# Performance work log

Measured on AMD Instinct MI355X. Metric: run time of the kernel, lower is better.

The kernel has to match this reference:

```python
import jax, jax.numpy as jnp
import numpy as np

H = 24        # attn.heads (Flux)
ENC = 512     # encoder (text) token count, hard-coded in the source via emb[:512]
EPS = 1e-6    # RMSNorm eps


def _rms(x, w):
    # RMSNorm over head_dim (Flux norm_q / norm_k)
    return x * jax.lax.rsqrt(jnp.mean(x * x, axis=-1, keepdims=True) + EPS) * w


def _rope(x, cos, sin):
    # diffusers apply_rotary_emb, use_real=True, unbind_dim=-1
    xr = x.reshape(x.shape[:-1] + (-1, 2))
    rot = jnp.stack([-xr[..., 1], xr[..., 0]], axis=-1).reshape(x.shape)
    return x * cos + rot * sin


def setup_inputs() -> dict:
    key = jax.random.key(0)
    ks = jax.random.split(key, 26)
    B, F, D = 2, 1024, 3072
    hd = D // H
    S = ENC + F
    lin = lambda k: 0.02 * jax.random.normal(k, (D, D), jnp.float32)
    bias = lambda k: 0.02 * jax.random.normal(k, (D,), jnp.float32)
    nw = lambda k: 1.0 + 0.02 * jax.random.normal(k, (hd,), jnp.float32)
    return {
        'hidden_states': jax.random.normal(ks[0], (B, F, D), jnp.float32),
        'encoder_hidden_states': jax.random.normal(ks[1], (B, ENC, D), jnp.float32),
        'rot_cos': jax.random.uniform(ks[2], (S, hd), jnp.float32, minval=-1.0, maxval=1.0),
        'rot_sin': jax.random.uniform(ks[3], (S, hd), jnp.float32, minval=-1.0, maxval=1.0),
        'wq': lin(ks[4]), 'bq': bias(ks[5]),
        'wk': lin(ks[6]), 'bk': bias(ks[7]),
        'wv': lin(ks[8]), 'bv': bias(ks[9]),
        'waq': lin(ks[10]), 'baq': bias(ks[11]),
        'wak': lin(ks[12]), 'bak': bias(ks[13]),
        'wav': lin(ks[14]), 'bav': bias(ks[15]),
        'wo': lin(ks[16]), 'bo': bias(ks[17]),
        'wao': lin(ks[18]), 'bao': bias(ks[19]),
        'nq': nw(ks[20]), 'nk': nw(ks[21]),
        'naq': nw(ks[22]), 'nak': nw(ks[23]),
    }


def reference(hidden_states, encoder_hidden_states, rot_cos, rot_sin,
              wq, bq, wk, bk, wv, bv, waq, baq, wak, bak, wav, bav,
              wo, bo, wao, bao, nq, nk, naq, nak):
    B, F, D = hidden_states.shape
    hd = D // H

    def proj(x, w, b):
        y = x @ w.T + b
        return y.reshape(x.shape[0], -1, H, hd).transpose(0, 2, 1, 3)  # [B,H,S,hd]

    q = _rms(proj(hidden_states, wq, bq), nq)   # [B,H,F,hd]
    k = _rms(proj(hidden_states, wk, bk), nk)
    v = proj(hidden_states, wv, bv)

    # cross-batch mixing: 'b h f d -> 1 h (b f) d' then repeat over batch
    k = jnp.broadcast_to(k.transpose(1, 0, 2, 3).reshape(1, H, B * F, hd), (B, H, B * F, hd))
    v = jnp.broadcast_to(v.transpose(1, 0, 2, 3).reshape(1, H, B * F, hd), (B, H, B * F, hd))

    # key rotary: encoder part once, image part repeated num_components times
    cos_k = jnp.concatenate([rot_cos[:ENC]] + [rot_cos[ENC:]] * B, axis=0)
    sin_k = jnp.concatenate([rot_sin[:ENC]] + [rot_sin[ENC:]] * B, axis=0)

    eq = _rms(proj(encoder_hidden_states, waq, baq), naq)  # [B,H,ENC,hd]
    ek = _rms(proj(encoder_hidden_states, wak, bak), nak)
    ev = proj(encoder_hidden_states, wav, bav)

    q = jnp.concatenate([eq, q], axis=2)  # [B,H,ENC+F,hd]
    k = jnp.concatenate([ek, k], axis=2)  # [B,H,ENC+B*F,hd]
    v = jnp.concatenate([ev, v], axis=2)

    q = _rope(q, rot_cos, rot_sin)
    k = _rope(k, cos_k, sin_k)

    scale = hd ** -0.5
    attn = jax.nn.softmax(jnp.einsum('bhqd,bhkd->bhqk', q, k) * scale, axis=-1)
    out = jnp.einsum('bhqk,bhkd->bhqd', attn, v)
    out = out.transpose(0, 2, 1, 3).reshape(B, -1, D)  # [B,ENC+F,D]

    enc_out = out[:, :ENC] @ wao.T + bao
    hs_out = out[:, ENC:] @ wo.T + bo
    return (hs_out, enc_out)
```

## Files before the change

### kernel.cpp

```cpp
#include <hip/hip_runtime.h>

typedef __attribute__((ext_vector_type(8))) short bf16x8;
typedef __attribute__((ext_vector_type(8))) unsigned short u16x8;
typedef __attribute__((ext_vector_type(4))) unsigned short u16x4;
typedef __attribute__((ext_vector_type(4))) float f32x4;

#define DEV static __device__ __forceinline__

DEV unsigned short f2bf(float f){
  unsigned u = __float_as_uint(f);
  u += 0x7fff + ((u>>16)&1);
  return (unsigned short)(u>>16);
}
DEV float bf2f(unsigned short b){ return __uint_as_float(((unsigned)b)<<16); }

DEV void gll16(const void* g, void* l){
  __builtin_amdgcn_global_load_lds((__attribute__((address_space(1))) unsigned*)(void*)g,
                                   (__attribute__((address_space(3))) unsigned*)l, 16, 0, 0);
}

__global__ void k_cast(const float* __restrict__ x, unsigned short* __restrict__ y, int n4){
  int i = blockIdx.x*256 + threadIdx.x;
  if (i >= n4) return;
  f32x4 v = ((const f32x4*)x)[i];
  u16x4 o = { f2bf(v.x), f2bf(v.y), f2bf(v.z), f2bf(v.w) };
  ((u16x4*)y)[i] = o;
}

__global__ __launch_bounds__(256) void k_gemm(
    const unsigned short* __restrict__ X, const unsigned short* __restrict__ W,
    unsigned short* __restrict__ Yb, float* __restrict__ Yf,
    const float* __restrict__ ba, const float* __restrict__ bb, const float* __restrict__ bc,
    int N, int K, int sec_nb, int tpb_log2, int stot, int soff)
{
  __shared__ unsigned short As[2][4096];
  __shared__ unsigned short Bs[2][4096];
  const int t = threadIdx.x, w = t>>6, l = t&63;
  const int by = blockIdx.y;
  const int wsel = (by >= 2*sec_nb) ? 2 : (by >= sec_nb ? 1 : 0);
  const int Cl = (by - wsel*sec_nb)*128;
  const unsigned short* Wp = W + (long)wsel*sec_nb*128*K;
  const float* bias = (wsel==0) ? ba : (wsel==1 ? bb : bc);
  const int R = blockIdx.x*128, C = by*128;
  const long xbase = (long)(R>>tpb_log2)*stot + soff + (R & ((1<<tpb_log2)-1));
  const int wr = w>>1, wc = w&1;
  f32x4 acc[4][4] = {};
  const int nk = K>>5;

  auto stage = [&](int buf, int kt){
    const int k0 = kt*32;
    #pragma unroll
    for (int c=0;c<2;c++){
      int row = c*64 + (t>>2);
      int scol = ((t&3)<<3) ^ ((row&3)<<3);
      gll16(X + (xbase+row)*K + k0 + scol, &As[buf][c*2048 + w*512]);
      gll16(Wp + (long)(Cl+row)*K + k0 + scol, &Bs[buf][c*2048 + w*512]);
    }
  };

  stage(0,0);
  int buf = 0;
  for (int kt=0; kt<nk; kt++){
    __syncthreads();
    if (kt+1 < nk) stage(buf^1, kt+1);
    bf16x8 a[4], b[4];
    #pragma unroll
    for (int m=0;m<4;m++){
      int ar = wr*64 + m*16 + (l&15);
      int ac = ((l>>4)<<3) ^ ((ar&3)<<3);
      a[m] = *(const bf16x8*)&As[buf][ar*32 + ac];
      int br = wc*64 + m*16 + (l&15);
      int bc2 = ((l>>4)<<3) ^ ((br&3)<<3);
      b[m] = *(const bf16x8*)&Bs[buf][br*32 + bc2];
    }
    #pragma unroll
    for (int m=0;m<4;m++)
      #pragma unroll
      for (int n=0;n<4;n++)
        acc[m][n] = __builtin_amdgcn_mfma_f32_16x16x32_bf16(a[m], b[n], acc[m][n], 0,0,0);
    buf ^= 1;
  }

  #pragma unroll
  for (int m=0;m<4;m++){
    int row = R + wr*64 + m*16 + ((l>>4)<<2);
    #pragma unroll
    for (int n=0;n<4;n++){
      int cl = wc*64 + n*16 + (l&15);
      float bvv = bias[Cl + cl];
      int col = C + cl;
      #pragma unroll
      for (int r=0;r<4;r++){
        float v = acc[m][n][r] + bvv;
        long idx = (long)(row+r)*N + col;
        if (Yf) Yf[idx] = v;
        else Yb[idx] = f2bf(v);
      }
    }
  }
}

__global__ __launch_bounds__(256) void k_gemmO(
    const unsigned short* __restrict__ X, const unsigned short* __restrict__ Wf,
    float* __restrict__ out, const float* __restrict__ bo, const float* __restrict__ bao)
{
  const int K = 3072;
  __shared__ unsigned short As[2][4096];
  __shared__ unsigned short Bs[2][4096];
  const int t = threadIdx.x, w = t>>6, l = t&63;
  const int bx = blockIdx.x, by = blockIdx.y;
  const bool enc = bx >= 16;
  const unsigned short* Wp = Wf + (enc ? 9437184 : 0);
  const float* bias = enc ? bao : bo;
  const int R = bx*128, C = by*128;
  long xbase, obase;
  if (!enc){ xbase = (long)(R>>10)*1536 + 512 + (R&1023); obase = (long)R*3072; }
  else { int Rp = R-2048; xbase = (long)(Rp>>9)*1536 + (Rp&511); obase = 6291456 + (long)Rp*3072; }
  const int wr = w>>1, wc = w&1;
  f32x4 acc[4][4] = {};

  auto stage = [&](int buf, int kt){
    const int k0 = kt*32;
    #pragma unroll
    for (int c=0;c<2;c++){
      int row = c*64 + (t>>2);
      int scol = ((t&3)<<3) ^ ((row&3)<<3);
      gll16(X + (xbase+row)*K + k0 + scol, &As[buf][c*2048 + w*512]);
      gll16(Wp + (long)(C+row)*K + k0 + scol, &Bs[buf][c*2048 + w*512]);
    }
  };

  stage(0,0);
  int buf = 0;
  for (int kt=0; kt<96; kt++){
    __syncthreads();
    if (kt+1 < 96) stage(buf^1, kt+1);
    bf16x8 a[4], b[4];
    #pragma unroll
    for (int m=0;m<4;m++){
      int ar = wr*64 + m*16 + (l&15);
      int ac = ((l>>4)<<3) ^ ((ar&3)<<3);
      a[m] = *(const bf16x8*)&As[buf][ar*32 + ac];
      int br = wc*64 + m*16 + (l&15);
      int bc2 = ((l>>4)<<3) ^ ((br&3)<<3);
      b[m] = *(const bf16x8*)&Bs[buf][br*32 + bc2];
    }
    #pragma unroll
    for (int m=0;m<4;m++)
      #pragma unroll
      for (int n=0;n<4;n++)
        acc[m][n] = __builtin_amdgcn_mfma_f32_16x16x32_bf16(a[m], b[n], acc[m][n], 0,0,0);
    buf ^= 1;
  }

  #pragma unroll
  for (int m=0;m<4;m++){
    int rl = wr*64 + m*16 + ((l>>4)<<2);
    #pragma unroll
    for (int n=0;n<4;n++){
      int col = C + wc*64 + n*16 + (l&15);
      float bvv = bias[col];
      #pragma unroll
      for (int r=0;r<4;r++)
        out[obase + (long)(rl+r)*3072 + col] = acc[m][n][r] + bvv;
    }
  }
}

__global__ void k_ppqk(const unsigned short* __restrict__ Y, int ystr, int yoff,
    const float* __restrict__ nw,
    const float* __restrict__ cs, const float* __restrict__ sn, unsigned short* __restrict__ dst,
    int T_log2, int tpb_log2, int dest_off, int S, int no_batch,
    int pos_off, int pos_mask, float qscale)
{
  int rid = blockIdx.x*4 + (threadIdx.x>>6);
  int l = threadIdx.x & 63;
  int h = rid >> T_log2, tk = rid & ((1<<T_log2)-1);
  unsigned pair = *(const unsigned*)(Y + (long)tk*ystr + yoff + h*128 + 2*l);
  float x0 = bf2f((unsigned short)(pair&0xffff));
  float x1 = bf2f((unsigned short)(pair>>16));
  float ss = x0*x0 + x1*x1;
  #pragma unroll
  for (int m=1;m<64;m<<=1) ss += __shfl_xor(ss, m);
  float rr = rsqrtf(ss*(1.0f/128.0f) + 1e-6f);
  x0 *= rr*nw[2*l]; x1 *= rr*nw[2*l+1];
  int p = pos_off + (tk & pos_mask);
  float c0 = cs[p*128 + 2*l], c1 = cs[p*128 + 2*l+1];
  float s0 = sn[p*128 + 2*l], s1 = sn[p*128 + 2*l+1];
  float o0 = (x0*c0 - x1*s0)*qscale;
  float o1 = (x1*c1 + x0*s1)*qscale;
  long idx;
  if (no_batch) idx = (long)h*S + tk;
  else {
    int b = tk >> tpb_log2;
    int sq = dest_off + (tk & ((1<<tpb_log2)-1));
    idx = (long)(b*24+h)*S + sq;
  }
  unsigned out = (unsigned)f2bf(o0) | ((unsigned)f2bf(o1)<<16);
  *(unsigned*)(dst + idx*128 + 2*l) = out;
}

__global__ void k_ppv(const unsigned short* __restrict__ Y, int ystr, int yoff,
                      unsigned short* __restrict__ Vt, int vstr, int no_batch)
{
  __shared__ unsigned short tileS[64][136];
  int t = threadIdx.x, h = blockIdx.y;
  int tile0 = blockIdx.x*64;
  #pragma unroll
  for (int c=0;c<4;c++){
    int j = c*16 + (t>>4), col = (t&15)*8;
    *(u16x8*)&tileS[j][col] = *(const u16x8*)(Y + (long)(tile0+j)*ystr + yoff + h*128 + col);
  }
  __syncthreads();
  int d = t>>1, half = t&1;
  unsigned short tmp[32];
  #pragma unroll
  for (int i=0;i<32;i++) tmp[i] = tileS[half*32+i][d];
  long base;
  if (no_batch) base = ((long)h*128 + d)*vstr + tile0 + half*32;
  else { int b = tile0>>9; base = ((long)(b*24+h)*128 + d)*vstr + (tile0&511) + half*32; }
  #pragma unroll
  for (int k=0;k<4;k++) *(u16x8*)(Vt + base + k*8) = *(const u16x8*)&tmp[k*8];
}

__global__ __launch_bounds__(256) void k_attn(
    const unsigned short* __restrict__ Q,
    const unsigned short* __restrict__ Ke, const unsigned short* __restrict__ Ki,
    const unsigned short* __restrict__ Ve, const unsigned short* __restrict__ Vi,
    unsigned short* __restrict__ AO)
{
  __shared__ unsigned short Ks[8192];
  __shared__ unsigned short Vs[8192];
  __shared__ unsigned short Ps[4][1408];
  const int t = threadIdx.x, w = t>>6, l = t&63;
  const int h = blockIdx.y, b = blockIdx.z;
  const int bh = b*24 + h;
  const int q0 = blockIdx.x*64 + w*16;

  bf16x8 qf[4];
  {
    const unsigned short* qp = Q + ((long)bh*1536 + q0 + (l&15))*128 + ((l>>4)<<3);
    #pragma unroll
    for (int kc=0;kc<4;kc++) qf[kc] = *(const bf16x8*)(qp + kc*32);
  }
  f32x4 o[8] = {};
  float mx[4] = {-1e30f,-1e30f,-1e30f,-1e30f};
  float ls[4] = {0,0,0,0};

  for (int jt=0; jt<40; jt++){
    const unsigned short *ksrc, *vsrc; int vstr;
    if (jt < 8){
      ksrc = Ke + ((long)bh*512 + jt*64)*128;
      vsrc = Ve + (long)bh*65536 + jt*64;
      vstr = 512;
    } else {
      ksrc = Ki + ((long)h*2048 + (jt-8)*64)*128;
      vsrc = Vi + (long)h*262144 + (jt-8)*64;
      vstr = 2048;
    }
    #pragma unroll
    for (int c=0;c<4;c++){
      int row = c*16 + (t>>4);
      int col = ((t&15)<<3) ^ ((row&7)<<3);
      gll16(ksrc + row*128 + col, &Ks[c*2048 + w*512]);
    }
    #pragma unroll
    for (int c=0;c<4;c++){
      int row = c*32 + (t>>3);
      int col = ((t&7)<<3) ^ ((row&7)<<3);
      gll16(vsrc + (long)row*vstr + col, &Vs[c*2048 + w*512]);
    }
    __syncthreads();

    f32x4 sf[4];
    __builtin_amdgcn_s_setprio(1);
    #pragma unroll
    for (int ct=0;ct<4;ct++){
      f32x4 s = {};
      #pragma unroll
      for (int kc=0;kc<4;kc++){
        int krow = ct*16 + (l&15);
        int kcol = (kc*32 + ((l>>4)<<3)) ^ ((krow&7)<<3);
        bf16x8 kb = *(const bf16x8*)&Ks[krow*128 + kcol];
        s = __builtin_amdgcn_mfma_f32_16x16x32_bf16(qf[kc], kb, s, 0,0,0);
      }
      sf[ct] = s;
    }
    __builtin_amdgcn_s_setprio(0);

    float pm[4]; int ok = 1;
    #pragma unroll
    for (int r=0;r<4;r++){
      pm[r] = fmaxf(fmaxf(sf[0][r],sf[1][r]), fmaxf(sf[2][r],sf[3][r]));
      ok &= (pm[r] <= mx[r] + 8.0f);
    }
    if (!__all(ok)){
      #pragma unroll
      for (int r=0;r<4;r++){
        float tmax = pm[r];
        #pragma unroll
        for (int m=1;m<16;m<<=1) tmax = fmaxf(tmax, __shfl_xor(tmax, m));
        float mn = fmaxf(mx[r], tmax);
        float al = exp2f(mx[r]-mn);
        mx[r] = mn;
        ls[r] *= al;
        #pragma unroll
        for (int f=0;f<8;f++) o[f][r] *= al;
      }
    }
    #pragma unroll
    for (int ct=0;ct<4;ct++){
      #pragma unroll
      for (int r=0;r<4;r++){
        float pv = exp2f(sf[ct][r]-mx[r]);
        ls[r] += pv;
        int prow = ((l>>4)<<2) + r;
        Ps[w][prow*88 + ct*16 + (l&15)] = f2bf(pv);
      }
    }
    bf16x8 pa[2];
    #pragma unroll
    for (int kc=0;kc<2;kc++)
      pa[kc] = *(const bf16x8*)&Ps[w][(l&15)*88 + kc*32 + ((l>>4)<<3)];
    __builtin_amdgcn_s_setprio(1);
    #pragma unroll
    for (int f=0;f<8;f++){
      #pragma unroll
      for (int kc=0;kc<2;kc++){
        int vrow = f*16 + (l&15);
        int vcol = (kc*32 + ((l>>4)<<3)) ^ ((vrow&7)<<3);
        bf16x8 vb = *(const bf16x8*)&Vs[vrow*64 + vcol];
        o[f] = __builtin_amdgcn_mfma_f32_16x16x32_bf16(pa[kc], vb, o[f], 0,0,0);
      }
    }
    __builtin_amdgcn_s_setprio(0);
    __syncthreads();
  }

  #pragma unroll
  for (int r=0;r<4;r++){
    #pragma unroll
    for (int m=1;m<16;m<<=1) ls[r] += __shfl_xor(ls[r], m);
  }
  #pragma unroll
  for (int r=0;r<4;r++){
    int qrow = q0 + ((l>>4)<<2) + r;
    float inv = 1.0f/ls[r];
    #pragma unroll
    for (int f=0;f<8;f++){
      AO[((long)b*1536 + qrow)*3072 + h*128 + f*16 + (l&15)] = f2bf(o[f][r]*inv);
    }
  }
}

extern "C" void kernel_launch(void* const* d_in, const int* in_sizes, int n_in,
                              void* d_out, int out_size, void* d_ws, size_t ws_size,
                              hipStream_t stream)
{
  const float* hs  = (const float*)d_in[0];
  const float* ehs = (const float*)d_in[1];
  const float* rc  = (const float*)d_in[2];
  const float* rs_ = (const float*)d_in[3];
  const float* wq = (const float*)d_in[4];  const float* bq = (const float*)d_in[5];
  const float* wk = (const float*)d_in[6];  const float* bk = (const float*)d_in[7];
  const float* wv = (const float*)d_in[8];  const float* bv = (const float*)d_in[9];
  const float* waq= (const float*)d_in[10]; const float* baq= (const float*)d_in[11];
  const float* wak= (const float*)d_in[12]; const float* bak= (const float*)d_in[13];
  const float* wav= (const float*)d_in[14]; const float* bav= (const float*)d_in[15];
  const float* wo = (const float*)d_in[16]; const float* bo = (const float*)d_in[17];
  const float* wao= (const float*)d_in[18]; const float* bao= (const float*)d_in[19];
  const float* nq = (const float*)d_in[20]; const float* nk = (const float*)d_in[21];
  const float* naq= (const float*)d_in[22]; const float* nak= (const float*)d_in[23];

  const float qsc = (float)(0.08838834764831845 * 1.4426950408889634);

  char* p = (char*)d_ws;
  auto alloc = [&](size_t bytes){ char* r = p; p += bytes; return r; };

  if (ws_size >= (size_t)169869312){
    unsigned short* Xh = (unsigned short*)alloc(12582912);
    unsigned short* Xe = (unsigned short*)alloc(6291456);
    unsigned short* Wb = (unsigned short*)alloc(56623104);
    unsigned short* Yb = (unsigned short*)alloc(37748736);
    unsigned short* Qb = (unsigned short*)alloc(18874368);
    unsigned short* Ke = (unsigned short*)alloc(6291456);
    unsigned short* Ki = (unsigned short*)alloc(12582912);
    unsigned short* Ve = (unsigned short*)alloc(6291456);
    unsigned short* Vi = (unsigned short*)alloc(12582912);
    unsigned short* AO = Xh;

    k_cast<<<6144,256,0,stream>>>(hs, Xh, 1572864);
    k_cast<<<3072,256,0,stream>>>(ehs, Xe, 786432);

    k_cast<<<9216,256,0,stream>>>(wq, Wb, 2359296);
    k_cast<<<9216,256,0,stream>>>(wk, Wb + 9437184, 2359296);
    k_cast<<<9216,256,0,stream>>>(wv, Wb + 18874368, 2359296);
    k_gemm<<<dim3(16,72),256,0,stream>>>(Xh, Wb, Yb, nullptr, bq, bk, bv, 9216,3072, 24, 20,0,0);
    k_ppqk<<<12288,256,0,stream>>>(Yb, 9216, 0,    nq, rc, rs_, Qb, 11, 10, 512, 1536, 0, 512, 1023, qsc);
    k_ppqk<<<12288,256,0,stream>>>(Yb, 9216, 3072, nk, rc, rs_, Ki, 11, 0,  0,   2048, 1, 512, 1023, 1.0f);
    k_ppv<<<dim3(32,24),256,0,stream>>>(Yb, 9216, 6144, Vi, 2048, 1);

    k_cast<<<9216,256,0,stream>>>(waq, Wb, 2359296);
    k_cast<<<9216,256,0,stream>>>(wak, Wb + 9437184, 2359296);
    k_cast<<<9216,256,0,stream>>>(wav, Wb + 18874368, 2359296);
    k_gemm<<<dim3(8,72),256,0,stream>>>(Xe, Wb, Yb, nullptr, baq, bak, bav, 9216,3072, 24, 20,0,0);
    k_ppqk<<<6144,256,0,stream>>>(Yb, 9216, 0,    naq, rc, rs_, Qb, 10, 9, 0, 1536, 0, 0, 511, qsc);
    k_ppqk<<<6144,256,0,stream>>>(Yb, 9216, 3072, nak, rc, rs_, Ke, 10, 9, 0, 512,  0, 0, 511, 1.0f);
    k_ppv<<<dim3(16,24),256,0,stream>>>(Yb, 9216, 6144, Ve, 512, 0);

    k_attn<<<dim3(24,24,2),256,0,stream>>>(Qb, Ke, Ki, Ve, Vi, AO);

    k_cast<<<9216,256,0,stream>>>(wo,  Wb, 2359296);
    k_cast<<<9216,256,0,stream>>>(wao, Wb + 9437184, 2359296);
    k_gemmO<<<dim3(24,24),256,0,stream>>>(AO, Wb, (float*)d_out, bo, bao);
  } else {
    unsigned short* Xh = (unsigned short*)alloc(12582912);
    unsigned short* Xe = (unsigned short*)alloc(6291456);
    unsigned short* Wb = (unsigned short*)alloc(18874368);
    unsigned short* Yb = (unsigned short*)alloc(12582912);
    unsigned short* Qb = (unsigned short*)alloc(18874368);
    unsigned short* Ke = (unsigned short*)alloc(6291456);
    unsigned short* Ki = (unsigned short*)alloc(12582912);
    unsigned short* Ve = (unsigned short*)alloc(6291456);
    unsigned short* Vi = (unsigned short*)alloc(12582912);
    unsigned short* AO = Xh;

    k_cast<<<6144,256,0,stream>>>(hs, Xh, 1572864);
    k_cast<<<3072,256,0,stream>>>(ehs, Xe, 786432);
    auto cW = [&](const float* ww){ k_cast<<<9216,256,0,stream>>>(ww, Wb, 2359296); };

    cW(wq);
    k_gemm<<<dim3(16,24),256,0,stream>>>(Xh, Wb, Yb, nullptr, bq,bq,bq, 3072,3072, 24, 20,0,0);
    k_ppqk<<<12288,256,0,stream>>>(Yb, 3072, 0, nq, rc, rs_, Qb, 11, 10, 512, 1536, 0, 512, 1023, qsc);
    cW(wk);
    k_gemm<<<dim3(16,24),256,0,stream>>>(Xh, Wb, Yb, nullptr, bk,bk,bk, 3072,3072, 24, 20,0,0);
    k_ppqk<<<12288,256,0,stream>>>(Yb, 3072, 0, nk, rc, rs_, Ki, 11, 0, 0, 2048, 1, 512, 1023, 1.0f);
    cW(wv);
    k_gemm<<<dim3(16,24),256,0,stream>>>(Xh, Wb, Yb, nullptr, bv,bv,bv, 3072,3072, 24, 20,0,0);
    k_ppv<<<dim3(32,24),256,0,stream>>>(Yb, 3072, 0, Vi, 2048, 1);

    cW(waq);
    k_gemm<<<dim3(8,24),256,0,stream>>>(Xe, Wb, Yb, nullptr, baq,baq,baq, 3072,3072, 24, 20,0,0);
    k_ppqk<<<6144,256,0,stream>>>(Yb, 3072, 0, naq, rc, rs_, Qb, 10, 9, 0, 1536, 0, 0, 511, qsc);
    cW(wak);
    k_gemm<<<dim3(8,24),256,0,stream>>>(Xe, Wb, Yb, nullptr, bak,bak,bak, 3072,3072, 24, 20,0,0);
    k_ppqk<<<6144,256,0,stream>>>(Yb, 3072, 0, nak, rc, rs_, Ke, 10, 9, 0, 512, 0, 0, 511, 1.0f);
    cW(wav);
    k_gemm<<<dim3(8,24),256,0,stream>>>(Xe, Wb, Yb, nullptr, bav,bav,bav, 3072,3072, 24, 20,0,0);
    k_ppv<<<dim3(16,24),256,0,stream>>>(Yb, 3072, 0, Ve, 512, 0);

    k_attn<<<dim3(24,24,2),256,0,stream>>>(Qb, Ke, Ki, Ve, Vi, AO);

    cW(wo);
    k_gemm<<<dim3(16,24),256,0,stream>>>(AO, Wb, nullptr, (float*)d_out, bo,bo,bo, 3072,3072, 24, 10, 1536, 512);
    cW(wao);
    k_gemm<<<dim3(8,24),256,0,stream>>>(AO, Wb, nullptr, (float*)d_out + 6291456, bao,bao,bao, 3072,3072, 24, 9, 1536, 0);
  }
}
```

Before: 710.8 us.

## Fuse image and encoder QKV GEMMs into one launch and double-buffer attention K tiles

```diff
diff --git a/kernel.cpp b/kernel.cpp
--- a/kernel.cpp
+++ b/kernel.cpp
@@ -27,25 +27,40 @@
   ((u16x4*)y)[i] = o;
 }
 
-__global__ __launch_bounds__(256) void k_gemm(
-    const unsigned short* __restrict__ X, const unsigned short* __restrict__ W,
-    unsigned short* __restrict__ Yb, float* __restrict__ Yf,
-    const float* __restrict__ ba, const float* __restrict__ bb, const float* __restrict__ bc,
-    int N, int K, int sec_nb, int tpb_log2, int stot, int soff)
-{
+__global__ void k_castW(const float* __restrict__ s0, const float* __restrict__ s1,
+                        const float* __restrict__ s2, const float* __restrict__ s3,
+                        const float* __restrict__ s4, const float* __restrict__ s5,
+                        unsigned short* __restrict__ y){
+  unsigned i = blockIdx.x*256 + threadIdx.x;
+  unsigned seg = i / 2359296u;
+  unsigned off = i - seg*2359296u;
+  const float* s = seg==0?s0: seg==1?s1: seg==2?s2: seg==3?s3: seg==4?s4: s5;
+  f32x4 v = ((const f32x4*)s)[off];
+  u16x4 o = { f2bf(v.x), f2bf(v.y), f2bf(v.z), f2bf(v.w) };
+  ((u16x4*)y)[i] = o;
+}
+
+__global__ __launch_bounds__(256) void k_gemmQKV(
+    const unsigned short* __restrict__ X,
+    const unsigned short* __restrict__ Wimg, const unsigned short* __restrict__ Wenc,
+    unsigned short* __restrict__ Y,
+    const float* __restrict__ b0, const float* __restrict__ b1, const float* __restrict__ b2,
+    const float* __restrict__ b3, const float* __restrict__ b4, const float* __restrict__ b5,
+    int rows_img)
+{
+  const int K = 3072, N = 9216;
   __shared__ unsigned short As[2][4096];
   __shared__ unsigned short Bs[2][4096];
   const int t = threadIdx.x, w = t>>6, l = t&63;
   const int by = blockIdx.y;
-  const int wsel = (by >= 2*sec_nb) ? 2 : (by >= sec_nb ? 1 : 0);
-  const int Cl = (by - wsel*sec_nb)*128;
-  const unsigned short* Wp = W + (long)wsel*sec_nb*128*K;
-  const float* bias = (wsel==0) ? ba : (wsel==1 ? bb : bc);
-  const int R = blockIdx.x*128, C = by*128;
-  const long xbase = (long)(R>>tpb_log2)*stot + soff + (R & ((1<<tpb_log2)-1));
+  const int sec = by>=48 ? 2 : (by>=24 ? 1 : 0);
+  const int Cl = (by - sec*24)*128;
+  const int R = blockIdx.x*128;
+  const bool enc = (R >= rows_img);
+  const unsigned short* Wp = (enc ? Wenc : Wimg) + (long)sec*9437184 + (long)Cl*K;
+  const float* bias = enc ? (sec==0?b3: sec==1?b4: b5) : (sec==0?b0: sec==1?b1: b2);
   const int wr = w>>1, wc = w&1;
   f32x4 acc[4][4] = {};
-  const int nk = K>>5;
 
   auto stage = [&](int buf, int kt){
     const int k0 = kt*32;
@@ -53,16 +68,16 @@
     for (int c=0;c<2;c++){
       int row = c*64 + (t>>2);
       int scol = ((t&3)<<3) ^ ((row&3)<<3);
-      gll16(X + (xbase+row)*K + k0 + scol, &As[buf][c*2048 + w*512]);
-      gll16(Wp + (long)(Cl+row)*K + k0 + scol, &Bs[buf][c*2048 + w*512]);
+      gll16(X + (long)(R+row)*K + k0 + scol, &As[buf][c*2048 + w*512]);
+      gll16(Wp + (long)row*K + k0 + scol, &Bs[buf][c*2048 + w*512]);
     }
   };
 
   stage(0,0);
   int buf = 0;
-  for (int kt=0; kt<nk; kt++){
+  for (int kt=0; kt<96; kt++){
     __syncthreads();
-    if (kt+1 < nk) stage(buf^1, kt+1);
+    if (kt+1 < 96) stage(buf^1, kt+1);
     bf16x8 a[4], b[4];
     #pragma unroll
     for (int m=0;m<4;m++){
@@ -88,14 +103,10 @@
     for (int n=0;n<4;n++){
       int cl = wc*64 + n*16 + (l&15);
       float bvv = bias[Cl + cl];
-      int col = C + cl;
-      #pragma unroll
-      for (int r=0;r<4;r++){
-        float v = acc[m][n][r] + bvv;
-        long idx = (long)(row+r)*N + col;
-        if (Yf) Yf[idx] = v;
-        else Yb[idx] = f2bf(v);
-      }
+      long col = (long)by*128 + cl;
+      #pragma unroll
+      for (int r=0;r<4;r++)
+        Y[(long)(row+r)*N + col] = f2bf(acc[m][n][r] + bvv);
     }
   }
 }
@@ -229,7 +240,7 @@
     const unsigned short* __restrict__ Ve, const unsigned short* __restrict__ Vi,
     unsigned short* __restrict__ AO)
 {
-  __shared__ unsigned short Ks[8192];
+  __shared__ unsigned short Ks[2][8192];
   __shared__ unsigned short Vs[8192];
   __shared__ unsigned short Ps[4][1408];
   const int t = threadIdx.x, w = t>>6, l = t&63;
@@ -237,41 +248,45 @@
   const int bh = b*24 + h;
   const int q0 = blockIdx.x*64 + w*16;
 
-  bf16x8 qf[4];
-  {
-    const unsigned short* qp = Q + ((long)bh*1536 + q0 + (l&15))*128 + ((l>>4)<<3);
-    #pragma unroll
-    for (int kc=0;kc<4;kc++) qf[kc] = *(const bf16x8*)(qp + kc*32);
-  }
-  f32x4 o[8] = {};
-  float mx[4] = {-1e30f,-1e30f,-1e30f,-1e30f};
-  float ls[4] = {0,0,0,0};
-
-  for (int jt=0; jt<40; jt++){
-    const unsigned short *ksrc, *vsrc; int vstr;
-    if (jt < 8){
-      ksrc = Ke + ((long)bh*512 + jt*64)*128;
-      vsrc = Ve + (long)bh*65536 + jt*64;
-      vstr = 512;
-    } else {
-      ksrc = Ki + ((long)h*2048 + (jt-8)*64)*128;
-      vsrc = Vi + (long)h*262144 + (jt-8)*64;
-      vstr = 2048;
-    }
+  auto stageK = [&](int bufi, int jt){
+    const unsigned short* ksrc = (jt < 8) ? Ke + ((long)bh*512 + jt*64)*128
+                                          : Ki + ((long)h*2048 + (jt-8)*64)*128;
     #pragma unroll
     for (int c=0;c<4;c++){
       int row = c*16 + (t>>4);
       int col = ((t&15)<<3) ^ ((row&7)<<3);
-      gll16(ksrc + row*128 + col, &Ks[c*2048 + w*512]);
-    }
+      gll16(ksrc + row*128 + col, &Ks[bufi][c*2048 + w*512]);
+    }
+  };
+  auto stageV = [&](int jt){
+    const unsigned short* vsrc; long vstr;
+    if (jt < 8){ vsrc = Ve + (long)bh*65536 + jt*64; vstr = 512; }
+    else { vsrc = Vi + (long)h*262144 + (jt-8)*64; vstr = 2048; }
     #pragma unroll
     for (int c=0;c<4;c++){
       int row = c*32 + (t>>3);
       int col = ((t&7)<<3) ^ ((row&7)<<3);
       gll16(vsrc + (long)row*vstr + col, &Vs[c*2048 + w*512]);
     }
+  };
+
+  bf16x8 qf[4];
+  {
+    const unsigned short* qp = Q + ((long)bh*1536 + q0 + (l&15))*128 + ((l>>4)<<3);
+    #pragma unroll
+    for (int kc=0;kc<4;kc++) qf[kc] = *(const bf16x8*)(qp + kc*32);
+  }
+  f32x4 o[8] = {};
+  float mx[4] = {-1e30f,-1e30f,-1e30f,-1e30f};
+  float ls[4] = {0,0,0,0};
+
+  stageK(0, 0);
+  for (int jt=0; jt<40; jt++){
     __syncthreads();
-
+    stageV(jt);
+    if (jt+1 < 40) stageK((jt+1)&1, jt+1);
+
+    const unsigned short* Kb = Ks[jt&1];
     f32x4 sf[4];
     __builtin_amdgcn_s_setprio(1);
     #pragma unroll
@@ -281,7 +296,7 @@
       for (int kc=0;kc<4;kc++){
         int krow = ct*16 + (l&15);
         int kcol = (kc*32 + ((l>>4)<<3)) ^ ((krow&7)<<3);
-        bf16x8 kb = *(const bf16x8*)&Ks[krow*128 + kcol];
+        bf16x8 kb = *(const bf16x8*)&Kb[krow*128 + kcol];
         s = __builtin_amdgcn_mfma_f32_16x16x32_bf16(qf[kc], kb, s, 0,0,0);
       }
       sf[ct] = s;
@@ -318,6 +333,8 @@
         Ps[w][prow*88 + ct*16 + (l&15)] = f2bf(pv);
       }
     }
+    __syncthreads();
+
     bf16x8 pa[2];
     #pragma unroll
     for (int kc=0;kc<2;kc++)
@@ -334,7 +351,6 @@
       }
     }
     __builtin_amdgcn_s_setprio(0);
-    __syncthreads();
   }
 
   #pragma unroll
@@ -377,7 +393,39 @@
   char* p = (char*)d_ws;
   auto alloc = [&](size_t bytes){ char* r = p; p += bytes; return r; };
 
-  if (ws_size >= (size_t)169869312){
+  if (ws_size >= (size_t)245366784){
+    unsigned short* Xh = (unsigned short*)alloc(12582912);
+    unsigned short* Xe = (unsigned short*)alloc(6291456);
+    unsigned short* Wb = (unsigned short*)alloc(113246208);
+    unsigned short* Yb = (unsigned short*)alloc(56623104);
+    unsigned short* Qb = (unsigned short*)alloc(18874368);
+    unsigned short* Ke = (unsigned short*)alloc(6291456);
+    unsigned short* Ki = (unsigned short*)alloc(12582912);
+    unsigned short* Ve = (unsigned short*)alloc(6291456);
+    unsigned short* Vi = (unsigned short*)alloc(12582912);
+    unsigned short* AO = Xh;
+
+    k_cast<<<6144,256,0,stream>>>(hs, Xh, 1572864);
+    k_cast<<<3072,256,0,stream>>>(ehs, Xe, 786432);
+    k_castW<<<55296,256,0,stream>>>(wq, wk, wv, waq, wak, wav, Wb);
+
+    k_gemmQKV<<<dim3(24,72),256,0,stream>>>(Xh, Wb, Wb + 28311552, Yb,
+                                            bq, bk, bv, baq, bak, bav, 2048);
+
+    unsigned short* Ye = Yb + (long)18874368;
+    k_ppqk<<<12288,256,0,stream>>>(Yb, 9216, 0,    nq,  rc, rs_, Qb, 11, 10, 512, 1536, 0, 512, 1023, qsc);
+    k_ppqk<<<12288,256,0,stream>>>(Yb, 9216, 3072, nk,  rc, rs_, Ki, 11, 0,  0,   2048, 1, 512, 1023, 1.0f);
+    k_ppv<<<dim3(32,24),256,0,stream>>>(Yb, 9216, 6144, Vi, 2048, 1);
+    k_ppqk<<<6144,256,0,stream>>>(Ye, 9216, 0,    naq, rc, rs_, Qb, 10, 9, 0, 1536, 0, 0, 511, qsc);
+    k_ppqk<<<6144,256,0,stream>>>(Ye, 9216, 3072, nak, rc, rs_, Ke, 10, 9, 0, 512,  0, 0, 511, 1.0f);
+    k_ppv<<<dim3(16,24),256,0,stream>>>(Ye, 9216, 6144, Ve, 512, 0);
+
+    k_attn<<<dim3(24,24,2),256,0,stream>>>(Qb, Ke, Ki, Ve, Vi, AO);
+
+    k_cast<<<9216,256,0,stream>>>(wo,  Wb, 2359296);
+    k_cast<<<9216,256,0,stream>>>(wao, Wb + 9437184, 2359296);
+    k_gemmO<<<dim3(24,24),256,0,stream>>>(AO, Wb, (float*)d_out, bo, bao);
+  } else {
     unsigned short* Xh = (unsigned short*)alloc(12582912);
     unsigned short* Xe = (unsigned short*)alloc(6291456);
     unsigned short* Wb = (unsigned short*)alloc(56623104);
@@ -395,7 +443,8 @@
     k_cast<<<9216,256,0,stream>>>(wq, Wb, 2359296);
     k_cast<<<9216,256,0,stream>>>(wk, Wb + 9437184, 2359296);
     k_cast<<<9216,256,0,stream>>>(wv, Wb + 18874368, 2359296);
-    k_gemm<<<dim3(16,72),256,0,stream>>>(Xh, Wb, Yb, nullptr, bq, bk, bv, 9216,3072, 24, 20,0,0);
+    k_gemmQKV<<<dim3(16,72),256,0,stream>>>(Xh, Wb, Wb, Yb,
+                                            bq, bk, bv, bq, bk, bv, 1<<28);
     k_ppqk<<<12288,256,0,stream>>>(Yb, 9216, 0,    nq, rc, rs_, Qb, 11, 10, 512, 1536, 0, 512, 1023, qsc);
     k_ppqk<<<12288,256,0,stream>>>(Yb, 9216, 3072, nk, rc, rs_, Ki, 11, 0,  0,   2048, 1, 512, 1023, 1.0f);
     k_ppv<<<dim3(32,24),256,0,stream>>>(Yb, 9216, 6144, Vi, 2048, 1);
@@ -403,7 +452,8 @@
     k_cast<<<9216,256,0,stream>>>(waq, Wb, 2359296);
     k_cast<<<9216,256,0,stream>>>(wak, Wb + 9437184, 2359296);
     k_cast<<<9216,256,0,stream>>>(wav, Wb + 18874368, 2359296);
-    k_gemm<<<dim3(8,72),256,0,stream>>>(Xe, Wb, Yb, nullptr, baq, bak, bav, 9216,3072, 24, 20,0,0);
+    k_gemmQKV<<<dim3(8,72),256,0,stream>>>(Xe, Wb, Wb, Yb,
+                                           baq, bak, bav, baq, bak, bav, 0);
     k_ppqk<<<6144,256,0,stream>>>(Yb, 9216, 0,    naq, rc, rs_, Qb, 10, 9, 0, 1536, 0, 0, 511, qsc);
     k_ppqk<<<6144,256,0,stream>>>(Yb, 9216, 3072, nak, rc, rs_, Ke, 10, 9, 0, 512,  0, 0, 511, 1.0f);
     k_ppv<<<dim3(16,24),256,0,stream>>>(Yb, 9216, 6144, Ve, 512, 0);
@@ -413,47 +463,5 @@
     k_cast<<<9216,256,0,stream>>>(wo,  Wb, 2359296);
     k_cast<<<9216,256,0,stream>>>(wao, Wb + 9437184, 2359296);
     k_gemmO<<<dim3(24,24),256,0,stream>>>(AO, Wb, (float*)d_out, bo, bao);
-  } else {
-    unsigned short* Xh = (unsigned short*)alloc(12582912);
-    unsigned short* Xe = (unsigned short*)alloc(6291456);
-    unsigned short* Wb = (unsigned short*)alloc(18874368);
-    unsigned short* Yb = (unsigned short*)alloc(12582912);
-    unsigned short* Qb = (unsigned short*)alloc(18874368);
-    unsigned short* Ke = (unsigned short*)alloc(6291456);
-    unsigned short* Ki = (unsigned short*)alloc(12582912);
-    unsigned short* Ve = (unsigned short*)alloc(6291456);
-    unsigned short* Vi = (unsigned short*)alloc(12582912);
-    unsigned short* AO = Xh;
-
-    k_cast<<<6144,256,0,stream>>>(hs, Xh, 1572864);
-    k_cast<<<3072,256,0,stream>>>(ehs, Xe, 786432);
-    auto cW = [&](const float* ww){ k_cast<<<9216,256,0,stream>>>(ww, Wb, 2359296); };
-
-    cW(wq);
-    k_gemm<<<dim3(16,24),256,0,stream>>>(Xh, Wb, Yb, nullptr, bq,bq,bq, 3072,3072, 24, 20,0,0);
-    k_ppqk<<<12288,256,0,stream>>>(Yb, 3072, 0, nq, rc, rs_, Qb, 11, 10, 512, 1536, 0, 512, 1023, qsc);
-    cW(wk);
-    k_gemm<<<dim3(16,24),256,0,stream>>>(Xh, Wb, Yb, nullptr, bk,bk,bk, 3072,3072, 24, 20,0,0);
-    k_ppqk<<<12288,256,0,stream>>>(Yb, 3072, 0, nk, rc, rs_, Ki, 11, 0, 0, 2048, 1, 512, 1023, 1.0f);
-    cW(wv);
-    k_gemm<<<dim3(16,24),256,0,stream>>>(Xh, Wb, Yb, nullptr, bv,bv,bv, 3072,3072, 24, 20,0,0);
-    k_ppv<<<dim3(32,24),256,0,stream>>>(Yb, 3072, 0, Vi, 2048, 1);
-
-    cW(waq);
-    k_gemm<<<dim3(8,24),256,0,stream>>>(Xe, Wb, Yb, nullptr, baq,baq,baq, 3072,3072, 24, 20,0,0);
-    k_ppqk<<<6144,256,0,stream>>>(Yb, 3072, 0, naq, rc, rs_, Qb, 10, 9, 0, 1536, 0, 0, 511, qsc);
-    cW(wak);
-    k_gemm<<<dim3(8,24),256,0,stream>>>(Xe, Wb, Yb, nullptr, bak,bak,bak, 3072,3072, 24, 20,0,0);
-    k_ppqk<<<6144,256,0,stream>>>(Yb, 3072, 0, nak, rc, rs_, Ke, 10, 9, 0, 512, 0, 0, 511, 1.0f);
-    cW(wav);
-    k_gemm<<<dim3(8,24),256,0,stream>>>(Xe, Wb, Yb, nullptr, bav,bav,bav, 3072,3072, 24, 20,0,0);
-    k_ppv<<<dim3(16,24),256,0,stream>>>(Yb, 3072, 0, Ve, 512, 0);
-
-    k_attn<<<dim3(24,24,2),256,0,stream>>>(Qb, Ke, Ki, Ve, Vi, AO);
-
-    cW(wo);
-    k_gemm<<<dim3(16,24),256,0,stream>>>(AO, Wb, nullptr, (float*)d_out, bo,bo,bo, 3072,3072, 24, 10, 1536, 512);
-    cW(wao);
-    k_gemm<<<dim3(8,24),256,0,stream>>>(AO, Wb, nullptr, (float*)d_out + 6291456, bao,bao,bao, 3072,3072, 24, 9, 1536, 0);
-  }
-}
+  }
+}
```

Result: slower. 744.9 us (+4.8%).
